# Performance work log

Hardware: AMD Instinct MI355X
Metric: run time of the kernel (lower is better)

The kernel has to match this reference:

```python
import jax, jax.numpy as jnp
import numpy as np

EPS = 1e-12  # torch F.normalize eps

def l2_normalize(x):
    n = jnp.sqrt(jnp.sum(x * x, axis=-1, keepdims=True))
    return x / jnp.maximum(n, EPS)

def entmax15(z):
    # Exact 1.5-entmax (Peters & Martins 2019), rowwise over last dim.
    z = z / 2.0
    z_srt = jnp.flip(jnp.sort(z, axis=-1), axis=-1)  # descending
    k = jnp.arange(1, z.shape[-1] + 1, dtype=z.dtype)
    mean = jnp.cumsum(z_srt, axis=-1) / k
    mean_sq = jnp.cumsum(z_srt * z_srt, axis=-1) / k
    ss = k * (mean_sq - mean * mean)
    delta = jnp.clip((1.0 - ss) / k, 0.0, None)
    tau = mean - jnp.sqrt(delta)
    support = (tau <= z_srt).astype(jnp.int32)
    k_star = jnp.sum(support, axis=-1, keepdims=True)  # support size >= 1
    tau_star = jnp.take_along_axis(tau, k_star - 1, axis=-1)
    p = jnp.clip(z - tau_star, 0.0, None)
    return p * p

def setup_inputs() -> dict:
    key = jax.random.key(0)
    ks = jax.random.split(key, 4)
    E, S, H, P = 8192, 8192, 512, 64
    lim = float(np.sqrt(6.0 / (H + P)))  # xavier_uniform bound
    return {
        "edge_repr": jax.random.normal(ks[0], (E, H), dtype=jnp.float32),
        "sub_repr": jax.random.normal(ks[1], (S, H), dtype=jnp.float32),
        "W_sub": jax.random.uniform(ks[2], (P, H), jnp.float32, -lim, lim),
        "b_sub": jnp.zeros((P,), jnp.float32),
        "W_edge": jax.random.uniform(ks[3], (P, H), jnp.float32, -lim, lim),
        "b_edge": jnp.zeros((P,), jnp.float32),
        "log_scale": jnp.asarray(np.log(5.0), jnp.float32),
    }

def reference(edge_repr, sub_repr, W_sub, b_sub, W_edge, b_edge, log_scale):
    sub_proj = l2_normalize(sub_repr @ W_sub.T + b_sub)    # [S, P]
    edge_proj = l2_normalize(edge_repr @ W_edge.T + b_edge)  # [E, P]
    scale = jnp.clip(jnp.exp(log_scale), 0.5, 20.0)
    scores = (sub_proj @ edge_proj.T) * scale  # [S, E]
    return entmax15(scores)
```

## Files before the change

### kernel.cpp

```cpp
#include <hip/hip_runtime.h>
#include <hip/hip_fp16.h>
#include <math.h>

#define ITERS 12

typedef __attribute__((ext_vector_type(8))) short short8;
typedef __attribute__((ext_vector_type(4))) float float4v;

static __device__ inline unsigned short f2bf(float f) {
    union { float f; unsigned int u; } c; c.f = f;
    unsigned int u = c.u;
    u += 0x7fffu + ((u >> 16) & 1u);
    return (unsigned short)(u >> 16);
}
static __device__ inline float bf2f(unsigned short h) {
    union { float f; unsigned int u; } c; c.u = ((unsigned int)h) << 16;
    return c.f;
}

__global__ __launch_bounds__(256) void proj_norm_kernel(
    const float* __restrict__ Xsub, const float* __restrict__ Xedge,
    const float* __restrict__ Wsub, const float* __restrict__ bsub,
    const float* __restrict__ Wedge, const float* __restrict__ bedge,
    unsigned short* __restrict__ subE, unsigned short* __restrict__ edgeE)
{
    const int mat = blockIdx.y;
    const float* X  = mat ? Xedge : Xsub;
    const float* W  = mat ? Wedge : Wsub;
    const float* Bv = mat ? bedge : bsub;
    unsigned short* OUT = mat ? edgeE : subE;

    const int r0 = blockIdx.x * 32;
    const int t  = threadIdx.x;
    const int tx = t & 15, ty = t >> 4;

    __shared__ float xs[64 * 34];
    __shared__ float ws[64 * 68];

    float acc[2][4] = {};

    for (int ch = 0; ch < 8; ++ch) {
        const int kb = ch * 64;
#pragma unroll
        for (int i = 0; i < 2; ++i) {
            int e = t + 256 * i;
            int row = e & 31, kq = e >> 5;
            float4 xv = *(const float4*)(X + (size_t)(r0 + row) * 512 + kb + kq * 4);
            xs[(kq * 4 + 0) * 34 + row] = xv.x;
            xs[(kq * 4 + 1) * 34 + row] = xv.y;
            xs[(kq * 4 + 2) * 34 + row] = xv.z;
            xs[(kq * 4 + 3) * 34 + row] = xv.w;
        }
#pragma unroll
        for (int i = 0; i < 4; ++i) {
            int e = t + 256 * i;
            int col = e & 63, kq = e >> 6;
            float4 wv = *(const float4*)(W + (size_t)col * 512 + kb + kq * 4);
            ws[(kq * 4 + 0) * 68 + col] = wv.x;
            ws[(kq * 4 + 1) * 68 + col] = wv.y;
            ws[(kq * 4 + 2) * 68 + col] = wv.z;
            ws[(kq * 4 + 3) * 68 + col] = wv.w;
        }
        __syncthreads();
#pragma unroll 8
        for (int k = 0; k < 64; ++k) {
            const float2 a2 = *(const float2*)&xs[k * 34 + ty * 2];
            const float4 b4 = *(const float4*)&ws[k * 68 + tx * 4];
            acc[0][0] = fmaf(a2.x, b4.x, acc[0][0]);
            acc[0][1] = fmaf(a2.x, b4.y, acc[0][1]);
            acc[0][2] = fmaf(a2.x, b4.z, acc[0][2]);
            acc[0][3] = fmaf(a2.x, b4.w, acc[0][3]);
            acc[1][0] = fmaf(a2.y, b4.x, acc[1][0]);
            acc[1][1] = fmaf(a2.y, b4.y, acc[1][1]);
            acc[1][2] = fmaf(a2.y, b4.z, acc[1][2]);
            acc[1][3] = fmaf(a2.y, b4.w, acc[1][3]);
        }
        __syncthreads();
    }

    const float4 bb = *(const float4*)(Bv + tx * 4);
#pragma unroll
    for (int i = 0; i < 2; ++i) {
        acc[i][0] += bb.x; acc[i][1] += bb.y; acc[i][2] += bb.z; acc[i][3] += bb.w;
        float s = acc[i][0]*acc[i][0] + acc[i][1]*acc[i][1]
                + acc[i][2]*acc[i][2] + acc[i][3]*acc[i][3];
#pragma unroll
        for (int off = 1; off <= 8; off <<= 1)
            s += __shfl_xor(s, off, 64);
        const float inv = 1.0f / fmaxf(sqrtf(s), 1e-12f);

        unsigned short h[4], l[4];
#pragma unroll
        for (int j = 0; j < 4; ++j) {
            const float v = acc[i][j] * inv;
            h[j] = f2bf(v);
            l[j] = f2bf(v - bf2f(h[j]));
        }
        uint2 hp, lp;
        hp.x = (unsigned)h[0] | ((unsigned)h[1] << 16);
        hp.y = (unsigned)h[2] | ((unsigned)h[3] << 16);
        lp.x = (unsigned)l[0] | ((unsigned)l[1] << 16);
        lp.y = (unsigned)l[2] | ((unsigned)l[3] << 16);

        unsigned short* base = OUT + (size_t)(r0 + ty * 2 + i) * 192 + tx * 4;
        *(uint2*)(base)       = hp;
        *(uint2*)(base + 64)  = mat ? hp : lp;
        *(uint2*)(base + 128) = mat ? lp : hp;
    }
}

__global__ __launch_bounds__(256, 4) void score_mfma_kernel(
    const unsigned short* __restrict__ subE,
    const unsigned short* __restrict__ edgeE,
    const float* __restrict__ log_scale, __half* __restrict__ z)
{
    const int t    = threadIdx.x;
    const int lane = t & 63;
    const int wid  = t >> 6;
    const int li   = lane & 15;
    const int quad = lane >> 4;
    const int s0   = blockIdx.y * 128;
    const int e0   = blockIdx.x * 64;
    const int mrow0 = (wid & 1) * 64;
    const int ncol0 = (wid >> 1) * 32;

    __shared__ unsigned short aS[128 * 72];
    __shared__ unsigned short bS[64 * 72];

    float4v acc[4][2];
#pragma unroll
    for (int mi = 0; mi < 4; ++mi)
#pragma unroll
        for (int ni = 0; ni < 2; ++ni)
            acc[mi][ni] = (float4v){0.f, 0.f, 0.f, 0.f};

    for (int c = 0; c < 3; ++c) {
        if (c) __syncthreads();
#pragma unroll
        for (int i = 0; i < 4; ++i) {
            int e = t + 256 * i;
            int row = e >> 3, off = e & 7;
            *(float4*)&aS[row * 72 + off * 8] =
                *(const float4*)(subE + (size_t)(s0 + row) * 192 + c * 64 + off * 8);
        }
#pragma unroll
        for (int i = 0; i < 2; ++i) {
            int e = t + 256 * i;
            int row = e >> 3, off = e & 7;
            *(float4*)&bS[row * 72 + off * 8] =
                *(const float4*)(edgeE + (size_t)(e0 + row) * 192 + c * 64 + off * 8);
        }
        __syncthreads();

#pragma unroll
        for (int ks = 0; ks < 2; ++ks) {
            short8 af[4], bf[2];
#pragma unroll
            for (int mi = 0; mi < 4; ++mi)
                af[mi] = *(const short8*)&aS[(mrow0 + mi * 16 + li) * 72 + ks * 32 + quad * 8];
#pragma unroll
            for (int ni = 0; ni < 2; ++ni)
                bf[ni] = *(const short8*)&bS[(ncol0 + ni * 16 + li) * 72 + ks * 32 + quad * 8];
#pragma unroll
            for (int mi = 0; mi < 4; ++mi)
#pragma unroll
                for (int ni = 0; ni < 2; ++ni)
                    acc[mi][ni] = __builtin_amdgcn_mfma_f32_16x16x32_bf16(
                        af[mi], bf[ni], acc[mi][ni], 0, 0, 0);
        }
    }

    float sc = expf(log_scale[0]);
    sc = fminf(fmaxf(sc, 0.5f), 20.0f);
    const float zs = sc * 0.5f;

#pragma unroll
    for (int mi = 0; mi < 4; ++mi)
#pragma unroll
        for (int ni = 0; ni < 2; ++ni) {
            const int col = e0 + ncol0 + ni * 16 + li;
#pragma unroll
            for (int reg = 0; reg < 4; ++reg) {
                const int row = s0 + mrow0 + mi * 16 + quad * 4 + reg;
                z[(size_t)row * 8192 + col] = __float2half_rn(acc[mi][ni][reg] * zs);
            }
        }
}

__global__ __launch_bounds__(256) void entmax_fp16_kernel(
    const __half* __restrict__ z, float* __restrict__ out)
{
    const int row  = blockIdx.x;
    const int t    = threadIdx.x;
    const int lane = t & 63, wid = t >> 6;
    const __half* zr = z + (size_t)row * 8192;

    float4 rd[4];
#pragma unroll
    for (int c = 0; c < 4; ++c)
        rd[c] = *(const float4*)(zr + c * 2048 + t * 8);

    float zv[32];
#pragma unroll
    for (int c = 0; c < 4; ++c) {
        const __half2* p = (const __half2*)&rd[c];
#pragma unroll
        for (int j = 0; j < 4; ++j) {
            float2 f2 = __half22float2(p[j]);
            zv[c * 8 + j * 2 + 0] = f2.x;
            zv[c * 8 + j * 2 + 1] = f2.y;
        }
    }

    __shared__ float tblm[4];
    __shared__ float tbl[2][4][3];

    float m = -1e30f;
#pragma unroll
    for (int i = 0; i < 32; ++i) m = fmaxf(m, zv[i]);
#pragma unroll
    for (int off = 32; off; off >>= 1) m = fmaxf(m, __shfl_xor(m, off, 64));
    if (lane == 0) tblm[wid] = m;
    __syncthreads();
    m = fmaxf(fmaxf(tblm[0], tblm[1]), fmaxf(tblm[2], tblm[3]));

    float tau = m - 1.0f;

    for (int it = 0; it < ITERS; ++it) {
        float n = 0.f, s1 = 0.f, s2 = 0.f;
#pragma unroll
        for (int i = 0; i < 32; ++i) {
            const float e_  = zv[i];
            const bool  p_  = e_ > tau;
            const float zm_ = p_ ? e_ : 0.0f;
            n  += p_ ? 1.0f : 0.0f;
            s1 += zm_;
            s2  = fmaf(zm_, e_, s2);
        }
#pragma unroll
        for (int off = 32; off; off >>= 1) {
            n  += __shfl_xor(n,  off, 64);
            s1 += __shfl_xor(s1, off, 64);
            s2 += __shfl_xor(s2, off, 64);
        }
        if (lane == 0) {
            tbl[it & 1][wid][0] = n;
            tbl[it & 1][wid][1] = s1;
            tbl[it & 1][wid][2] = s2;
        }
        __syncthreads();
        float N = 0.f, S1 = 0.f, S2 = 0.f;
#pragma unroll
        for (int w = 0; w < 4; ++w) {
            N  += tbl[it & 1][w][0];
            S1 += tbl[it & 1][w][1];
            S2 += tbl[it & 1][w][2];
        }
        const float disc = S1 * S1 - N * (S2 - 1.0f);
        float tn;
        if (disc >= 0.0f) {
            tn = (S1 - sqrtf(disc)) / N;
        } else {
            const float g = S1 - N * tau;
            const float f = S2 - tau * (2.0f * S1 - N * tau);
            tn = tau + (f - 1.0f) / (2.0f * g);
        }
        if (tn == tau) break;
        tau = tn;
    }

#pragma unroll
    for (int c = 0; c < 4; ++c) {
        float4 p0, p1; float d;
        d = fmaxf(zv[c*8+0] - tau, 0.f); p0.x = d * d;
        d = fmaxf(zv[c*8+1] - tau, 0.f); p0.y = d * d;
        d = fmaxf(zv[c*8+2] - tau, 0.f); p0.z = d * d;
        d = fmaxf(zv[c*8+3] - tau, 0.f); p0.w = d * d;
        d = fmaxf(zv[c*8+4] - tau, 0.f); p1.x = d * d;
        d = fmaxf(zv[c*8+5] - tau, 0.f); p1.y = d * d;
        d = fmaxf(zv[c*8+6] - tau, 0.f); p1.z = d * d;
        d = fmaxf(zv[c*8+7] - tau, 0.f); p1.w = d * d;
        float* op = out + (size_t)row * 8192 + c * 2048 + t * 8;
        *(float4*)op       = p0;
        *(float4*)(op + 4) = p1;
    }
}

extern "C" void kernel_launch(void* const* d_in, const int* in_sizes, int n_in,
                              void* d_out, int out_size, void* d_ws, size_t ws_size,
                              hipStream_t stream)
{
    const float* edge_repr = (const float*)d_in[0];
    const float* sub_repr  = (const float*)d_in[1];
    const float* W_sub     = (const float*)d_in[2];
    const float* b_sub     = (const float*)d_in[3];
    const float* W_edge    = (const float*)d_in[4];
    const float* b_edge    = (const float*)d_in[5];
    const float* log_scale = (const float*)d_in[6];
    float* out = (float*)d_out;

    unsigned short* subE  = (unsigned short*)d_ws;
    unsigned short* edgeE = subE + (size_t)8192 * 192;
    __half*         zbuf  = (__half*)(edgeE + (size_t)8192 * 192);

    proj_norm_kernel<<<dim3(256, 2), 256, 0, stream>>>(
        sub_repr, edge_repr, W_sub, b_sub, W_edge, b_edge, subE, edgeE);

    score_mfma_kernel<<<dim3(128, 64), 256, 0, stream>>>(
        subE, edgeE, log_scale, zbuf);

    entmax_fp16_kernel<<<8192, 256, 0, stream>>>(zbuf, out);
}
```

Before: 417.9 us.

## Fuse score GEMM and entmax into one kernel holding rows in registers

Merges the score MFMA kernel and the entmax kernel into a single kernel. Each 512-thread block computes 16 full score rows and keeps them as packed fp16 in registers, 128 dwords per thread. Entmax is then solved per row with a block-wide reduction and a shared convergence flag, and the probabilities are written with nontemporal stores. This removes the 128MB fp16 round trip through global memory and one launch. In exchange it uses heavy register pressure and only 512 blocks, it reads B fragments straight from global memory without LDS staging, and the threshold iteration keeps running until all 16 rows in a block have converged.

```diff
diff --git a/kernel.cpp b/kernel.cpp
--- a/kernel.cpp
+++ b/kernel.cpp
@@ -109,181 +109,179 @@
     }
 }
 
-__global__ __launch_bounds__(256, 4) void score_mfma_kernel(
+__global__ __launch_bounds__(512, 2) void fused_score_entmax_kernel(
     const unsigned short* __restrict__ subE,
     const unsigned short* __restrict__ edgeE,
-    const float* __restrict__ log_scale, __half* __restrict__ z)
+    const float* __restrict__ log_scale,
+    float* __restrict__ out)
 {
     const int t    = threadIdx.x;
     const int lane = t & 63;
     const int wid  = t >> 6;
     const int li   = lane & 15;
     const int quad = lane >> 4;
-    const int s0   = blockIdx.y * 128;
-    const int e0   = blockIdx.x * 64;
-    const int mrow0 = (wid & 1) * 64;
-    const int ncol0 = (wid >> 1) * 32;
-
-    __shared__ unsigned short aS[128 * 72];
-    __shared__ unsigned short bS[64 * 72];
-
-    float4v acc[4][2];
-#pragma unroll
-    for (int mi = 0; mi < 4; ++mi)
-#pragma unroll
-        for (int ni = 0; ni < 2; ++ni)
-            acc[mi][ni] = (float4v){0.f, 0.f, 0.f, 0.f};
-
-    for (int c = 0; c < 3; ++c) {
-        if (c) __syncthreads();
-#pragma unroll
-        for (int i = 0; i < 4; ++i) {
-            int e = t + 256 * i;
-            int row = e >> 3, off = e & 7;
-            *(float4*)&aS[row * 72 + off * 8] =
-                *(const float4*)(subE + (size_t)(s0 + row) * 192 + c * 64 + off * 8);
-        }
-#pragma unroll
-        for (int i = 0; i < 2; ++i) {
-            int e = t + 256 * i;
-            int row = e >> 3, off = e & 7;
-            *(float4*)&bS[row * 72 + off * 8] =
-                *(const float4*)(edgeE + (size_t)(e0 + row) * 192 + c * 64 + off * 8);
-        }
-        __syncthreads();
-
-#pragma unroll
-        for (int ks = 0; ks < 2; ++ks) {
-            short8 af[4], bf[2];
-#pragma unroll
-            for (int mi = 0; mi < 4; ++mi)
-                af[mi] = *(const short8*)&aS[(mrow0 + mi * 16 + li) * 72 + ks * 32 + quad * 8];
-#pragma unroll
-            for (int ni = 0; ni < 2; ++ni)
-                bf[ni] = *(const short8*)&bS[(ncol0 + ni * 16 + li) * 72 + ks * 32 + quad * 8];
-#pragma unroll
-            for (int mi = 0; mi < 4; ++mi)
-#pragma unroll
-                for (int ni = 0; ni < 2; ++ni)
-                    acc[mi][ni] = __builtin_amdgcn_mfma_f32_16x16x32_bf16(
-                        af[mi], bf[ni], acc[mi][ni], 0, 0, 0);
-        }
-    }
+    const int r0   = blockIdx.x * 16;
+    const int c0   = wid * 1024;
+
+    __shared__ float redS[8][16][4];
+    __shared__ float tauS[16];
+    __shared__ int   convS;
+
+    short8 af[6];
+#pragma unroll
+    for (int kk = 0; kk < 6; ++kk)
+        af[kk] = *(const short8*)(subE + (size_t)(r0 + li) * 192 + kk * 32 + quad * 8);
 
     float sc = expf(log_scale[0]);
     sc = fminf(fmaxf(sc, 0.5f), 20.0f);
     const float zs = sc * 0.5f;
 
-#pragma unroll
-    for (int mi = 0; mi < 4; ++mi)
-#pragma unroll
-        for (int ni = 0; ni < 2; ++ni) {
-            const int col = e0 + ncol0 + ni * 16 + li;
-#pragma unroll
-            for (int reg = 0; reg < 4; ++reg) {
-                const int row = s0 + mrow0 + mi * 16 + quad * 4 + reg;
-                z[(size_t)row * 8192 + col] = __float2half_rn(acc[mi][ni][reg] * zs);
-            }
-        }
-}
-
-__global__ __launch_bounds__(256) void entmax_fp16_kernel(
-    const __half* __restrict__ z, float* __restrict__ out)
-{
-    const int row  = blockIdx.x;
-    const int t    = threadIdx.x;
-    const int lane = t & 63, wid = t >> 6;
-    const __half* zr = z + (size_t)row * 8192;
-
-    float4 rd[4];
-#pragma unroll
-    for (int c = 0; c < 4; ++c)
-        rd[c] = *(const float4*)(zr + c * 2048 + t * 8);
-
-    float zv[32];
-#pragma unroll
-    for (int c = 0; c < 4; ++c) {
-        const __half2* p = (const __half2*)&rd[c];
-#pragma unroll
-        for (int j = 0; j < 4; ++j) {
-            float2 f2 = __half22float2(p[j]);
-            zv[c * 8 + j * 2 + 0] = f2.x;
-            zv[c * 8 + j * 2 + 1] = f2.y;
-        }
-    }
-
-    __shared__ float tblm[4];
-    __shared__ float tbl[2][4][3];
-
-    float m = -1e30f;
-#pragma unroll
-    for (int i = 0; i < 32; ++i) m = fmaxf(m, zv[i]);
-#pragma unroll
-    for (int off = 32; off; off >>= 1) m = fmaxf(m, __shfl_xor(m, off, 64));
-    if (lane == 0) tblm[wid] = m;
+    unsigned int zh[128];
+
+#pragma unroll
+    for (int tp = 0; tp < 32; ++tp) {
+        const unsigned short* b0p = edgeE + (size_t)(c0 + tp * 32 + li) * 192 + quad * 8;
+        const unsigned short* b1p = b0p + (size_t)16 * 192;
+        float4v a0 = (float4v){0.f, 0.f, 0.f, 0.f};
+        float4v a1 = (float4v){0.f, 0.f, 0.f, 0.f};
+#pragma unroll
+        for (int kk = 0; kk < 6; ++kk) {
+            short8 b0 = *(const short8*)(b0p + kk * 32);
+            a0 = __builtin_amdgcn_mfma_f32_16x16x32_bf16(af[kk], b0, a0, 0, 0, 0);
+        }
+#pragma unroll
+        for (int kk = 0; kk < 6; ++kk) {
+            short8 b1 = *(const short8*)(b1p + kk * 32);
+            a1 = __builtin_amdgcn_mfma_f32_16x16x32_bf16(af[kk], b1, a1, 0, 0, 0);
+        }
+#pragma unroll
+        for (int r = 0; r < 4; ++r) {
+            union { unsigned u; __half2 h2; } cv;
+            cv.h2.x = __float2half_rn(a0[r] * zs);
+            cv.h2.y = __float2half_rn(a1[r] * zs);
+            zh[tp * 4 + r] = cv.u;
+        }
+    }
+
+    float mx[4];
+#pragma unroll
+    for (int r = 0; r < 4; ++r) mx[r] = -1e30f;
+#pragma unroll
+    for (int j = 0; j < 128; ++j) {
+        union { unsigned u; __half2 h2; } cv; cv.u = zh[j];
+        float2 f = __half22float2(cv.h2);
+        mx[j & 3] = fmaxf(mx[j & 3], fmaxf(f.x, f.y));
+    }
+#pragma unroll
+    for (int off = 1; off <= 8; off <<= 1)
+#pragma unroll
+        for (int r = 0; r < 4; ++r)
+            mx[r] = fmaxf(mx[r], __shfl_xor(mx[r], off, 64));
+    if (li == 0) {
+#pragma unroll
+        for (int r = 0; r < 4; ++r) redS[wid][quad * 4 + r][0] = mx[r];
+    }
     __syncthreads();
-    m = fmaxf(fmaxf(tblm[0], tblm[1]), fmaxf(tblm[2], tblm[3]));
-
-    float tau = m - 1.0f;
+    if (t < 16) {
+        float m = redS[0][t][0];
+#pragma unroll
+        for (int w = 1; w < 8; ++w) m = fmaxf(m, redS[w][t][0]);
+        tauS[t] = m - 1.0f;
+    }
+    __syncthreads();
+    float tau[4];
+#pragma unroll
+    for (int r = 0; r < 4; ++r) tau[r] = tauS[quad * 4 + r];
 
     for (int it = 0; it < ITERS; ++it) {
-        float n = 0.f, s1 = 0.f, s2 = 0.f;
-#pragma unroll
-        for (int i = 0; i < 32; ++i) {
-            const float e_  = zv[i];
-            const bool  p_  = e_ > tau;
-            const float zm_ = p_ ? e_ : 0.0f;
-            n  += p_ ? 1.0f : 0.0f;
-            s1 += zm_;
-            s2  = fmaf(zm_, e_, s2);
-        }
-#pragma unroll
-        for (int off = 32; off; off >>= 1) {
-            n  += __shfl_xor(n,  off, 64);
-            s1 += __shfl_xor(s1, off, 64);
-            s2 += __shfl_xor(s2, off, 64);
-        }
-        if (lane == 0) {
-            tbl[it & 1][wid][0] = n;
-            tbl[it & 1][wid][1] = s1;
-            tbl[it & 1][wid][2] = s2;
+        float n[4]  = {0.f, 0.f, 0.f, 0.f};
+        float s1[4] = {0.f, 0.f, 0.f, 0.f};
+        float s2[4] = {0.f, 0.f, 0.f, 0.f};
+#pragma unroll
+        for (int j = 0; j < 128; ++j) {
+            union { unsigned u; __half2 h2; } cv; cv.u = zh[j];
+            float2 f = __half22float2(cv.h2);
+            const int r = j & 3;
+            {
+                const bool  p  = f.x > tau[r];
+                const float zm = p ? f.x : 0.f;
+                n[r]  += p ? 1.f : 0.f;
+                s1[r] += zm;
+                s2[r]  = fmaf(zm, f.x, s2[r]);
+            }
+            {
+                const bool  p  = f.y > tau[r];
+                const float zm = p ? f.y : 0.f;
+                n[r]  += p ? 1.f : 0.f;
+                s1[r] += zm;
+                s2[r]  = fmaf(zm, f.y, s2[r]);
+            }
+        }
+#pragma unroll
+        for (int off = 1; off <= 8; off <<= 1)
+#pragma unroll
+            for (int r = 0; r < 4; ++r) {
+                n[r]  += __shfl_xor(n[r],  off, 64);
+                s1[r] += __shfl_xor(s1[r], off, 64);
+                s2[r] += __shfl_xor(s2[r], off, 64);
+            }
+        if (li == 0) {
+#pragma unroll
+            for (int r = 0; r < 4; ++r) {
+                redS[wid][quad * 4 + r][0] = n[r];
+                redS[wid][quad * 4 + r][1] = s1[r];
+                redS[wid][quad * 4 + r][2] = s2[r];
+            }
         }
         __syncthreads();
-        float N = 0.f, S1 = 0.f, S2 = 0.f;
-#pragma unroll
-        for (int w = 0; w < 4; ++w) {
-            N  += tbl[it & 1][w][0];
-            S1 += tbl[it & 1][w][1];
-            S2 += tbl[it & 1][w][2];
-        }
-        const float disc = S1 * S1 - N * (S2 - 1.0f);
-        float tn;
-        if (disc >= 0.0f) {
-            tn = (S1 - sqrtf(disc)) / N;
-        } else {
-            const float g = S1 - N * tau;
-            const float f = S2 - tau * (2.0f * S1 - N * tau);
-            tn = tau + (f - 1.0f) / (2.0f * g);
-        }
-        if (tn == tau) break;
-        tau = tn;
-    }
-
-#pragma unroll
-    for (int c = 0; c < 4; ++c) {
-        float4 p0, p1; float d;
-        d = fmaxf(zv[c*8+0] - tau, 0.f); p0.x = d * d;
-        d = fmaxf(zv[c*8+1] - tau, 0.f); p0.y = d * d;
-        d = fmaxf(zv[c*8+2] - tau, 0.f); p0.z = d * d;
-        d = fmaxf(zv[c*8+3] - tau, 0.f); p0.w = d * d;
-        d = fmaxf(zv[c*8+4] - tau, 0.f); p1.x = d * d;
-        d = fmaxf(zv[c*8+5] - tau, 0.f); p1.y = d * d;
-        d = fmaxf(zv[c*8+6] - tau, 0.f); p1.z = d * d;
-        d = fmaxf(zv[c*8+7] - tau, 0.f); p1.w = d * d;
-        float* op = out + (size_t)row * 8192 + c * 2048 + t * 8;
-        *(float4*)op       = p0;
-        *(float4*)(op + 4) = p1;
-    }
+
+        bool cf = true;
+        if (t < 16) {
+            float N = 0.f, S1 = 0.f, S2 = 0.f;
+#pragma unroll
+            for (int w = 0; w < 8; ++w) {
+                N  += redS[w][t][0];
+                S1 += redS[w][t][1];
+                S2 += redS[w][t][2];
+            }
+            const float told = tauS[t];
+            const float disc = S1 * S1 - N * (S2 - 1.0f);
+            float tn;
+            if (disc >= 0.0f) {
+                tn = (S1 - sqrtf(disc)) / N;
+            } else {
+                const float g = S1 - N * told;
+                const float f = S2 - told * (2.0f * S1 - N * told);
+                tn = told + (f - 1.0f) / (2.0f * g);
+            }
+            cf = (tn == told);
+            tauS[t] = tn;
+        }
+        if (wid == 0) {
+            unsigned long long bm = __ballot(cf);
+            if (lane == 0) convS = (bm == ~0ull) ? 1 : 0;
+        }
+        __syncthreads();
+#pragma unroll
+        for (int r = 0; r < 4; ++r) tau[r] = tauS[quad * 4 + r];
+        if (convS) break;
+    }
+
+    float* orow[4];
+#pragma unroll
+    for (int r = 0; r < 4; ++r)
+        orow[r] = out + (size_t)(r0 + quad * 4 + r) * 8192 + c0 + li;
+#pragma unroll
+    for (int tp = 0; tp < 32; ++tp)
+#pragma unroll
+        for (int r = 0; r < 4; ++r) {
+            union { unsigned u; __half2 h2; } cv; cv.u = zh[tp * 4 + r];
+            float2 f = __half22float2(cv.h2);
+            float d0 = fmaxf(f.x - tau[r], 0.f);
+            float d1 = fmaxf(f.y - tau[r], 0.f);
+            __builtin_nontemporal_store(d0 * d0, orow[r] + tp * 32);
+            __builtin_nontemporal_store(d1 * d1, orow[r] + tp * 32 + 16);
+        }
 }
 
 extern "C" void kernel_launch(void* const* d_in, const int* in_sizes, int n_in,
@@ -301,13 +299,10 @@
 
     unsigned short* subE  = (unsigned short*)d_ws;
     unsigned short* edgeE = subE + (size_t)8192 * 192;
-    __half*         zbuf  = (__half*)(edgeE + (size_t)8192 * 192);
 
     proj_norm_kernel<<<dim3(256, 2), 256, 0, stream>>>(
         sub_repr, edge_repr, W_sub, b_sub, W_edge, b_edge, subE, edgeE);
 
-    score_mfma_kernel<<<dim3(128, 64), 256, 0, stream>>>(
-        subE, edgeE, log_scale, zbuf);
-
-    entmax_fp16_kernel<<<8192, 256, 0, stream>>>(zbuf, out);
-}
+    fused_score_entmax_kernel<<<dim3(512), 512, 0, stream>>>(
+        subE, edgeE, log_scale, out);
+}
```

New measurement: 713.4 us. 1.71x slower.
